# Optimization experiments

Measured on AMD Instinct MI355X. Metric: run time of the kernel, lower is better.

## Reference

```python
import jax, jax.numpy as jnp
import numpy as np

HID = 512
BATCH = 64
SRC_LEN = 2048


def setup_inputs() -> dict:
    key = jax.random.key(0)
    ks = jax.random.split(key, 8)
    s = 1.0 / np.sqrt(HID)
    return {
        "h": jax.random.normal(ks[0], (1, BATCH, HID), dtype=jnp.float32),
        "enc_out": jax.random.normal(ks[1], (BATCH, SRC_LEN, HID), dtype=jnp.float32),
        "W1_w": jax.random.uniform(ks[2], (HID, HID), jnp.float32, -s, s),
        "W1_b": jax.random.uniform(ks[3], (HID,), jnp.float32, -s, s),
        "W2_w": jax.random.uniform(ks[4], (HID, HID), jnp.float32, -s, s),
        "W2_b": jax.random.uniform(ks[5], (HID,), jnp.float32, -s, s),
        "V_w": jax.random.uniform(ks[6], (1, HID), jnp.float32, -s, s),
        "V_b": jax.random.uniform(ks[7], (1,), jnp.float32, -s, s),
    }


def reference(h, enc_out, W1_w, W1_b, W2_w, W2_b, V_w, V_b):
    # h: [1, B, H] -> [B, 1, H]; broadcast against enc_out: [B, S, H]
    h_b = jnp.transpose(h, (1, 0, 2))                       # [B, 1, H]
    proj_enc = jnp.einsum('bsh,oh->bso', enc_out, W1_w) + W1_b  # [B, S, H]
    proj_h = jnp.einsum('bqh,oh->bqo', h_b, W2_w) + W2_b        # [B, 1, H]
    energy = jnp.tanh(proj_enc + proj_h)                        # [B, S, H]
    scores = jnp.einsum('bsh,oh->bso', energy, V_w)[..., 0] + V_b[0]  # [B, S]
    return jax.nn.softmax(scores, axis=1)
```

## Files before the change

kernel.cpp:

```cpp
#include <hip/hip_runtime.h>
#include <hip/hip_bf16.h>

#define HID   512
#define BATCH 64
#define SRC   2048
#define MROWS (BATCH * SRC)

typedef __bf16 bf16x8 __attribute__((ext_vector_type(8)));
typedef __bf16 bf16x4 __attribute__((ext_vector_type(4)));
typedef float  f32x16 __attribute__((ext_vector_type(16)));

#define PANEL 520

__device__ inline float fast_tanh(float x) {
    float e = __builtin_amdgcn_exp2f(x * 2.8853900817779268f);
    return 1.0f - 2.0f * __builtin_amdgcn_rcpf(e + 1.0f);
}

template <int CTRL>
__device__ inline float dpp_add(float x) {
    int y = __builtin_amdgcn_update_dpp(0, __builtin_bit_cast(int, x), CTRL, 0xF, 0xF, true);
    return x + __builtin_bit_cast(float, y);
}

__device__ inline float reduce32(float x) {
    x = dpp_add<0xB1>(x);
    x = dpp_add<0x4E>(x);
    x = dpp_add<0x141>(x);
    x = dpp_add<0x140>(x);
    int y = __builtin_amdgcn_ds_swizzle(__builtin_bit_cast(int, x), 0x401F);
    return x + __builtin_bit_cast(float, y);
}

__global__ void prep(const float* __restrict__ W1w, __bf16* __restrict__ Bpk,
                     const float* __restrict__ h, const float* __restrict__ W2w,
                     const float* __restrict__ W2b, const float* __restrict__ W1b,
                     float* __restrict__ biasc) {
    __shared__ float hh[HID];
    int tid = threadIdx.x;
    if (blockIdx.x < 128) {
        int t = blockIdx.x * 256 + tid;
        int l = t & 63, tile = t >> 6;
        int ot = tile & 15, kt = tile >> 4;
        int o = ot * 32 + (l & 31);
        int k = kt * 16 + (l >> 5) * 8;
        const float* src = W1w + (size_t)o * HID + k;
        float4 v0 = *(const float4*)src;
        float4 v1 = *(const float4*)(src + 4);
        bf16x8 r;
        r[0]=(__bf16)v0.x; r[1]=(__bf16)v0.y; r[2]=(__bf16)v0.z; r[3]=(__bf16)v0.w;
        r[4]=(__bf16)v1.x; r[5]=(__bf16)v1.y; r[6]=(__bf16)v1.z; r[7]=(__bf16)v1.w;
        ((bf16x8*)Bpk)[t] = r;
    } else {
        int b = blockIdx.x - 128;
        hh[tid]       = h[b * HID + tid];
        hh[tid + 256] = h[b * HID + tid + 256];
        __syncthreads();
        const float4* h4 = (const float4*)hh;
        for (int o = tid; o < HID; o += 256) {
            const float4* w4 = (const float4*)(W2w + (size_t)o * HID);
            float s = 0.f;
            #pragma unroll 8
            for (int k = 0; k < HID / 4; ++k) {
                float4 a = h4[k]; float4 w = w4[k];
                s += a.x * w.x + a.y * w.y + a.z * w.z + a.w * w.w;
            }
            biasc[b * HID + o] = s + W2b[o] + W1b[o];
        }
    }
}

__global__ __launch_bounds__(512, 4) void attn_main(
        const float* __restrict__ enc, const __bf16* __restrict__ Bpk,
        const float* __restrict__ biasc, const float* __restrict__ Vw,
        float* __restrict__ scores) {
    __shared__ __bf16 AL[64 * PANEL];
    __shared__ float sred[64][9];

    const int tid = threadIdx.x;
    const int blockRow = blockIdx.x * 64;
    const int b = blockIdx.x >> 5;
    const int lane = tid & 63;
    const int wv = tid >> 6;
    const int col = lane & 31;
    const int hfi = lane >> 5;

    const int o0 = (2 * wv) * 32 + col;
    const int o1 = o0 + 32;
    float bb0 = biasc[b * HID + o0], bb1 = biasc[b * HID + o1];
    float vv0 = Vw[o0],               vv1 = Vw[o1];

    const float4* encB = (const float4*)enc + (size_t)blockRow * 128;
    #pragma unroll
    for (int i = 0; i < 16; ++i) {
        int f = i * 512 + tid;
        float4 v = encB[f];
        int row = f >> 7;
        int kq  = (f & 127) << 2;
        int kt = kq >> 4, half = (kq >> 3) & 1, j = kq & 7;
        int off = (kt * 2 + (row >> 5)) * PANEL + ((row & 31) + 32 * half) * 8 + j;
        bf16x4 o4;
        o4[0]=(__bf16)v.x; o4[1]=(__bf16)v.y; o4[2]=(__bf16)v.z; o4[3]=(__bf16)v.w;
        *(bf16x4*)&AL[off] = o4;
    }
    __syncthreads();

    const int rot = blockIdx.x & 31;
    const char* BpkB = (const char*)Bpk + (2 * wv) * 1024 + lane * 16;
    const __bf16* pA = AL + lane * 8;

    f32x16 acc00, acc01, acc10, acc11;
    #pragma unroll
    for (int i = 0; i < 16; ++i) { acc00[i]=0.f; acc01[i]=0.f; acc10[i]=0.f; acc11[i]=0.f; }

    bf16x8 b0 = *(const bf16x8*)(BpkB + (size_t)rot * 16384);
    bf16x8 b1 = *(const bf16x8*)(BpkB + (size_t)rot * 16384 + 1024);
    #pragma unroll 8
    for (int kt = 0; kt < 32; ++kt) {
        int in = (kt + 1 + rot) & 31;
        bf16x8 nb0 = *(const bf16x8*)(BpkB + (size_t)in * 16384);
        bf16x8 nb1 = *(const bf16x8*)(BpkB + (size_t)in * 16384 + 1024);
        int ia = (kt + rot) & 31;
        const __bf16* pa = pA + ia * (2 * PANEL);
        bf16x8 a0 = *(const bf16x8*)pa;
        bf16x8 a1 = *(const bf16x8*)(pa + PANEL);
        acc00 = __builtin_amdgcn_mfma_f32_32x32x16_bf16(a0, b0, acc00, 0, 0, 0);
        acc10 = __builtin_amdgcn_mfma_f32_32x32x16_bf16(a1, b0, acc10, 0, 0, 0);
        acc01 = __builtin_amdgcn_mfma_f32_32x32x16_bf16(a0, b1, acc01, 0, 0, 0);
        acc11 = __builtin_amdgcn_mfma_f32_32x32x16_bf16(a1, b1, acc11, 0, 0, 0);
        b0 = nb0; b1 = nb1;
    }

    #pragma unroll
    for (int r = 0; r < 16; ++r) {
        float p0 = vv0 * fast_tanh(acc00[r] + bb0) + vv1 * fast_tanh(acc01[r] + bb1);
        float p1 = vv0 * fast_tanh(acc10[r] + bb0) + vv1 * fast_tanh(acc11[r] + bb1);
        p0 = reduce32(p0);
        p1 = reduce32(p1);
        if (col == 0) {
            int rl = (r & 3) + 8 * (r >> 2) + 4 * hfi;
            sred[rl][wv]      = p0;
            sred[32 + rl][wv] = p1;
        }
    }
    __syncthreads();
    if (tid < 64) {
        float s = 0.f;
        #pragma unroll
        for (int w = 0; w < 8; ++w) s += sred[tid][w];
        scores[blockRow + tid] = s;
    }
}

__global__ void softmax_k(float* __restrict__ scores) {
    int b = blockIdx.x;
    int tid = threadIdx.x;
    int lane = tid & 63, wv = tid >> 6;
    __shared__ float red[4];
    float* row = scores + (size_t)b * SRC;
    float4 v0 = *(float4*)(row + tid * 8);
    float4 v1 = *(float4*)(row + tid * 8 + 4);
    float x[8] = {v0.x, v0.y, v0.z, v0.w, v1.x, v1.y, v1.z, v1.w};
    float mx = x[0];
    #pragma unroll
    for (int r = 1; r < 8; ++r) mx = fmaxf(mx, x[r]);
    #pragma unroll
    for (int m = 1; m <= 32; m <<= 1) mx = fmaxf(mx, __shfl_xor(mx, m, 64));
    if (lane == 0) red[wv] = mx;
    __syncthreads();
    mx = fmaxf(fmaxf(red[0], red[1]), fmaxf(red[2], red[3]));
    __syncthreads();
    float s = 0.f;
    #pragma unroll
    for (int r = 0; r < 8; ++r) {
        x[r] = __builtin_amdgcn_exp2f((x[r] - mx) * 1.44269504088896f);
        s += x[r];
    }
    #pragma unroll
    for (int m = 1; m <= 32; m <<= 1) s += __shfl_xor(s, m, 64);
    if (lane == 0) red[wv] = s;
    __syncthreads();
    s = red[0] + red[1] + red[2] + red[3];
    float inv = 1.0f / s;
    float4 o0 = make_float4(x[0] * inv, x[1] * inv, x[2] * inv, x[3] * inv);
    float4 o1 = make_float4(x[4] * inv, x[5] * inv, x[6] * inv, x[7] * inv);
    *(float4*)(row + tid * 8)     = o0;
    *(float4*)(row + tid * 8 + 4) = o1;
}

extern "C" void kernel_launch(void* const* d_in, const int* in_sizes, int n_in,
                              void* d_out, int out_size, void* d_ws, size_t ws_size,
                              hipStream_t stream) {
    const float* h    = (const float*)d_in[0];
    const float* enc  = (const float*)d_in[1];
    const float* W1w  = (const float*)d_in[2];
    const float* W1b  = (const float*)d_in[3];
    const float* W2w  = (const float*)d_in[4];
    const float* W2b  = (const float*)d_in[5];
    const float* Vw   = (const float*)d_in[6];
    float* out = (float*)d_out;

    __bf16* Bpk  = (__bf16*)d_ws;
    float*  biasc = (float*)((char*)d_ws + HID * HID * sizeof(__bf16));

    prep     <<<192, 256, 0, stream>>>(W1w, Bpk, h, W2w, W2b, W1b, biasc);
    attn_main<<<MROWS / 64, 512, 0, stream>>>(enc, Bpk, biasc, Vw, out);
    softmax_k<<<BATCH, 256, 0, stream>>>(out);
}
```

Baseline: 443.8 us.

## Double attention block row tile to 128 with 4x2 MFMA accumulators per wave

Each block now handles 128 encoder rows instead of 64, and each wave keeps 4x2 MFMA accumulator tiles, so every B (W1) fragment fetched from global memory is reused across twice as many rows. B fragments are double-buffered two k-steps ahead and issued before the encoder staging loop. Encoder loads become nontemporal, and the k rotation is staggered per block group. The trade-off is twice the LDS and more registers per block (launch bounds lowered to 2), so fewer blocks run per CU and there is less latency hiding for the large encoder stream.

```diff
diff --git a/kernel.cpp b/kernel.cpp
--- a/kernel.cpp
+++ b/kernel.cpp
@@ -9,6 +9,7 @@
 typedef __bf16 bf16x8 __attribute__((ext_vector_type(8)));
 typedef __bf16 bf16x4 __attribute__((ext_vector_type(4)));
 typedef float  f32x16 __attribute__((ext_vector_type(16)));
+typedef float  f32x4n __attribute__((ext_vector_type(4)));
 
 #define PANEL 520
 
@@ -70,16 +71,16 @@
     }
 }
 
-__global__ __launch_bounds__(512, 4) void attn_main(
+__global__ __launch_bounds__(512, 2) void attn_main(
         const float* __restrict__ enc, const __bf16* __restrict__ Bpk,
         const float* __restrict__ biasc, const float* __restrict__ Vw,
         float* __restrict__ scores) {
-    __shared__ __bf16 AL[64 * PANEL];
-    __shared__ float sred[64][9];
+    __shared__ __bf16 AL[128 * PANEL];
+    __shared__ float sred[128][9];
 
     const int tid = threadIdx.x;
-    const int blockRow = blockIdx.x * 64;
-    const int b = blockIdx.x >> 5;
+    const int blockRow = blockIdx.x * 128;
+    const int b = blockIdx.x >> 4;
     const int lane = tid & 63;
     const int wv = tid >> 6;
     const int col = lane & 31;
@@ -90,61 +91,79 @@
     float bb0 = biasc[b * HID + o0], bb1 = biasc[b * HID + o1];
     float vv0 = Vw[o0],               vv1 = Vw[o1];
 
-    const float4* encB = (const float4*)enc + (size_t)blockRow * 128;
-    #pragma unroll
-    for (int i = 0; i < 16; ++i) {
+    const int rot = (blockIdx.x + (blockIdx.x >> 3)) & 31;
+    const char* BpkB = (const char*)Bpk + (2 * wv) * 1024 + lane * 16;
+
+    bf16x8 bpre[2][2];
+    bpre[0][0] = *(const bf16x8*)(BpkB + (size_t)rot * 16384);
+    bpre[0][1] = *(const bf16x8*)(BpkB + (size_t)rot * 16384 + 1024);
+    int r1 = (rot + 1) & 31;
+    bpre[1][0] = *(const bf16x8*)(BpkB + (size_t)r1 * 16384);
+    bpre[1][1] = *(const bf16x8*)(BpkB + (size_t)r1 * 16384 + 1024);
+
+    const f32x4n* encB = (const f32x4n*)enc + (size_t)blockRow * 128;
+    #pragma unroll 8
+    for (int i = 0; i < 32; ++i) {
         int f = i * 512 + tid;
-        float4 v = encB[f];
+        f32x4n v = __builtin_nontemporal_load(encB + f);
         int row = f >> 7;
         int kq  = (f & 127) << 2;
         int kt = kq >> 4, half = (kq >> 3) & 1, j = kq & 7;
-        int off = (kt * 2 + (row >> 5)) * PANEL + ((row & 31) + 32 * half) * 8 + j;
+        int off = (kt * 4 + (row >> 5)) * PANEL + ((row & 31) + 32 * half) * 8 + j;
         bf16x4 o4;
         o4[0]=(__bf16)v.x; o4[1]=(__bf16)v.y; o4[2]=(__bf16)v.z; o4[3]=(__bf16)v.w;
         *(bf16x4*)&AL[off] = o4;
     }
-    __syncthreads();
-
-    const int rot = blockIdx.x & 31;
-    const char* BpkB = (const char*)Bpk + (2 * wv) * 1024 + lane * 16;
-    const __bf16* pA = AL + lane * 8;
-
-    f32x16 acc00, acc01, acc10, acc11;
-    #pragma unroll
-    for (int i = 0; i < 16; ++i) { acc00[i]=0.f; acc01[i]=0.f; acc10[i]=0.f; acc11[i]=0.f; }
-
-    bf16x8 b0 = *(const bf16x8*)(BpkB + (size_t)rot * 16384);
-    bf16x8 b1 = *(const bf16x8*)(BpkB + (size_t)rot * 16384 + 1024);
-    #pragma unroll 8
+
+    f32x16 acc[4][2];
+    #pragma unroll
+    for (int mt = 0; mt < 4; ++mt)
+        #pragma unroll
+        for (int i = 0; i < 16; ++i) { acc[mt][0][i] = 0.f; acc[mt][1][i] = 0.f; }
+
+    __syncthreads();
+
+    #pragma unroll 2
     for (int kt = 0; kt < 32; ++kt) {
-        int in = (kt + 1 + rot) & 31;
-        bf16x8 nb0 = *(const bf16x8*)(BpkB + (size_t)in * 16384);
-        bf16x8 nb1 = *(const bf16x8*)(BpkB + (size_t)in * 16384 + 1024);
+        const int cur = kt & 1;
+        bf16x8 ub0 = bpre[cur][0];
+        bf16x8 ub1 = bpre[cur][1];
+        int nk = (kt + 2 + rot) & 31;
+        bpre[cur][0] = *(const bf16x8*)(BpkB + (size_t)nk * 16384);
+        bpre[cur][1] = *(const bf16x8*)(BpkB + (size_t)nk * 16384 + 1024);
+
         int ia = (kt + rot) & 31;
-        const __bf16* pa = pA + ia * (2 * PANEL);
+        const __bf16* pa = AL + ia * (4 * PANEL) + lane * 8;
         bf16x8 a0 = *(const bf16x8*)pa;
         bf16x8 a1 = *(const bf16x8*)(pa + PANEL);
-        acc00 = __builtin_amdgcn_mfma_f32_32x32x16_bf16(a0, b0, acc00, 0, 0, 0);
-        acc10 = __builtin_amdgcn_mfma_f32_32x32x16_bf16(a1, b0, acc10, 0, 0, 0);
-        acc01 = __builtin_amdgcn_mfma_f32_32x32x16_bf16(a0, b1, acc01, 0, 0, 0);
-        acc11 = __builtin_amdgcn_mfma_f32_32x32x16_bf16(a1, b1, acc11, 0, 0, 0);
-        b0 = nb0; b1 = nb1;
-    }
-
-    #pragma unroll
-    for (int r = 0; r < 16; ++r) {
-        float p0 = vv0 * fast_tanh(acc00[r] + bb0) + vv1 * fast_tanh(acc01[r] + bb1);
-        float p1 = vv0 * fast_tanh(acc10[r] + bb0) + vv1 * fast_tanh(acc11[r] + bb1);
-        p0 = reduce32(p0);
-        p1 = reduce32(p1);
-        if (col == 0) {
-            int rl = (r & 3) + 8 * (r >> 2) + 4 * hfi;
-            sred[rl][wv]      = p0;
-            sred[32 + rl][wv] = p1;
+        bf16x8 a2 = *(const bf16x8*)(pa + 2 * PANEL);
+        bf16x8 a3 = *(const bf16x8*)(pa + 3 * PANEL);
+
+        acc[0][0] = __builtin_amdgcn_mfma_f32_32x32x16_bf16(a0, ub0, acc[0][0], 0, 0, 0);
+        acc[1][0] = __builtin_amdgcn_mfma_f32_32x32x16_bf16(a1, ub0, acc[1][0], 0, 0, 0);
+        acc[2][0] = __builtin_amdgcn_mfma_f32_32x32x16_bf16(a2, ub0, acc[2][0], 0, 0, 0);
+        acc[3][0] = __builtin_amdgcn_mfma_f32_32x32x16_bf16(a3, ub0, acc[3][0], 0, 0, 0);
+        acc[0][1] = __builtin_amdgcn_mfma_f32_32x32x16_bf16(a0, ub1, acc[0][1], 0, 0, 0);
+        acc[1][1] = __builtin_amdgcn_mfma_f32_32x32x16_bf16(a1, ub1, acc[1][1], 0, 0, 0);
+        acc[2][1] = __builtin_amdgcn_mfma_f32_32x32x16_bf16(a2, ub1, acc[2][1], 0, 0, 0);
+        acc[3][1] = __builtin_amdgcn_mfma_f32_32x32x16_bf16(a3, ub1, acc[3][1], 0, 0, 0);
+    }
+
+    #pragma unroll
+    for (int mt = 0; mt < 4; ++mt) {
+        #pragma unroll
+        for (int r = 0; r < 16; ++r) {
+            float p = vv0 * fast_tanh(acc[mt][0][r] + bb0)
+                    + vv1 * fast_tanh(acc[mt][1][r] + bb1);
+            p = reduce32(p);
+            if (col == 0) {
+                int rl = mt * 32 + (r & 3) + 8 * (r >> 2) + 4 * hfi;
+                sred[rl][wv] = p;
+            }
         }
     }
     __syncthreads();
-    if (tid < 64) {
+    if (tid < 128) {
         float s = 0.f;
         #pragma unroll
         for (int w = 0; w < 8; ++w) s += sred[tid][w];
@@ -204,6 +223,6 @@
     float*  biasc = (float*)((char*)d_ws + HID * HID * sizeof(__bf16));
 
     prep     <<<192, 256, 0, stream>>>(W1w, Bpk, h, W2w, W2b, W1b, biasc);
-    attn_main<<<MROWS / 64, 512, 0, stream>>>(enc, Bpk, biasc, Vw, out);
+    attn_main<<<MROWS / 128, 512, 0, stream>>>(enc, Bpk, biasc, Vw, out);
     softmax_k<<<BATCH, 256, 0, stream>>>(out);
 }
```

Measured after the change: 456.4 us. 1.03x slower.
